# Optimization experiments

Hardware: AMD Instinct MI355X
Metric: run time of the kernel (lower is better)

The kernel has to match this reference:

```python
import jax, jax.numpy as jnp
import numpy as np


def setup_inputs() -> dict:
    key = jax.random.key(0)
    kx, kw = jax.random.split(key)
    x = jax.random.normal(kx, (32, 128, 8192), dtype=jnp.float32)
    weight = jax.random.normal(kw, (128, 128, 1, 2), dtype=jnp.float32)
    return {"x": x, "weight": weight}


def reference(x, weight):
    # x: (bs, cin, d); weight: (cout, cin, 1, 2)
    bs, cin, d = x.shape
    xp = x.reshape(bs, cin, d // 2, 2)          # (bs, cin, d/2, 2)
    w = weight[:, :, 0, :]                      # (cout, cin, 2)
    # out[b, o, p] = sum_{c,k} x[b,c,p,k] * w[o,c,k] / sqrt(cin)
    out = jnp.einsum('bcpk,ock->bop', xp, w) / jnp.sqrt(jnp.float32(cin))
    return out
```

## Files before the change

### kernel.cpp

```cpp
#include <hip/hip_runtime.h>
#include <stdint.h>


typedef __attribute__((ext_vector_type(8))) short bf16x8;
typedef __attribute__((ext_vector_type(4))) float f32x4;

#define CIN  128
#define DLEN 8192
#define PLEN 4096
#define COUT 128

__device__ inline unsigned short f2bf(float f) {
    unsigned u = __builtin_bit_cast(unsigned, f);
    unsigned r = u + 0x7FFFu + ((u >> 16) & 1u);
    return (unsigned short)(r >> 16);
}

__device__ inline unsigned pack_bf(float a, float b) {
    unsigned ua = __builtin_bit_cast(unsigned, a);
    unsigned ub = __builtin_bit_cast(unsigned, b);
    unsigned ra = ua + 0x7FFFu + ((ua >> 16) & 1u);
    unsigned rb = ub + 0x7FFFu + ((ub >> 16) & 1u);
    return (ra >> 16) | (rb & 0xFFFF0000u);
}

__global__ __launch_bounds__(256) void convert_w(const float* __restrict__ w,
                                                 unsigned short* __restrict__ wb) {
    int t  = blockIdx.x * 256 + threadIdx.x;
    int o  = t >> 7;
    int k0 = (t & 127) * 2;
    const float scale = 0.088388347648318447f;
    float2 f = *(const float2*)(w + o * 256 + k0);
    unsigned v = (unsigned)f2bf(f.x * scale) | ((unsigned)f2bf(f.y * scale) << 16);
    int idx = (k0 >> 3) * 1024 + o * 8 + (k0 & 7);
    *(unsigned*)(wb + idx) = v;
}

__global__ __launch_bounds__(256, 4) void conv_mfma(const float* __restrict__ x,
                                                    const unsigned short* __restrict__ wb,
                                                    float* __restrict__ out) {
    int tile = blockIdx.x;
    int b    = tile >> 5;
    int pt   = (tile & 31) * 128;
    int lane = threadIdx.x & 63;
    int w    = threadIdx.x >> 6;
    int quad = lane >> 4;
    int l16  = lane & 15;
    int pbase = pt + w * 32;

    const float* xl = x + (size_t)b * ((size_t)CIN * DLEN)
                        + (size_t)(quad * 4) * DLEN + 2 * pbase + 4 * l16;
    const uint32_t* bb = (const uint32_t*)wb + quad * 512 + l16 * 4;

    f32x4 acc[2][8];
#pragma unroll
    for (int mt = 0; mt < 2; ++mt)
#pragma unroll
        for (int t = 0; t < 8; ++t)
            acc[mt][t] = (f32x4)(0.0f);

    float4 abuf[4];
#pragma unroll
    for (int jj = 0; jj < 4; ++jj)
        abuf[jj] = *(const float4*)(xl + (size_t)jj * DLEN);

#pragma unroll 1
    for (int kc = 0; kc < 8; ++kc) {
        union { bf16x8 v; unsigned uu[4]; } afr0, afr1;
#pragma unroll
        for (int jj = 0; jj < 4; ++jj) {
            afr0.uu[jj] = pack_bf(abuf[jj].x, abuf[jj].y);
            afr1.uu[jj] = pack_bf(abuf[jj].z, abuf[jj].w);
        }
        if (kc < 7) {
            const float* nx = xl + (size_t)((kc + 1) * 16) * DLEN;
#pragma unroll
            for (int jj = 0; jj < 4; ++jj)
                abuf[jj] = *(const float4*)(nx + (size_t)jj * DLEN);
        }
        const uint32_t* bk = bb + kc * 2048;
#pragma unroll
        for (int th = 0; th < 2; ++th) {
            union { bf16x8 v; uint4 u; } bfr[4];
#pragma unroll
            for (int tt = 0; tt < 4; ++tt)
                bfr[tt].u = *(const uint4*)(bk + (th * 4 + tt) * 64);
#pragma unroll
            for (int tt = 0; tt < 4; ++tt) {
                int t = th * 4 + tt;
                acc[0][t] = __builtin_amdgcn_mfma_f32_16x16x32_bf16(afr0.v, bfr[tt].v, acc[0][t], 0, 0, 0);
                acc[1][t] = __builtin_amdgcn_mfma_f32_16x16x32_bf16(afr1.v, bfr[tt].v, acc[1][t], 0, 0, 0);
            }
        }
    }

    float* ob = out + (size_t)b * ((size_t)COUT * PLEN) + pbase + quad * 8;
#pragma unroll
    for (int t = 0; t < 8; ++t) {
        int o = t * 16 + l16;
        float* orow = ob + (size_t)o * PLEN;
        f32x4 v0 = { acc[0][t][0], acc[1][t][0], acc[0][t][1], acc[1][t][1] };
        f32x4 v1 = { acc[0][t][2], acc[1][t][2], acc[0][t][3], acc[1][t][3] };
        *(f32x4*)(orow)     = v0;
        *(f32x4*)(orow + 4) = v1;
    }
}

extern "C" void kernel_launch(void* const* d_in, const int* in_sizes, int n_in,
                              void* d_out, int out_size, void* d_ws, size_t ws_size,
                              hipStream_t stream) {
    const float* x = (const float*)d_in[0];
    const float* w = (const float*)d_in[1];
    float* out = (float*)d_out;
    unsigned short* wb = (unsigned short*)d_ws;

    convert_w<<<64, 256, 0, stream>>>(w, wb);
    conv_mfma<<<1024, 256, 0, stream>>>(x, wb, out);
}
```

Baseline: 212.6 us.

## Fuse weight conversion into conv kernel, stage bf16 weights in LDS

Drops the separate weight-conversion kernel launch. Each block now converts the full fp32 weight matrix to scaled bf16 and stores it in 64KB of shared memory, then reads B fragments from LDS instead of global memory. Blocks grow to 512 threads covering 256 positions, halving the grid to 512 blocks. This saves one launch and the global weight reads, but every block repeats the conversion, and the larger LDS footprint may limit how many blocks fit per CU.

```diff
diff --git a/kernel.cpp b/kernel.cpp
--- a/kernel.cpp
+++ b/kernel.cpp
@@ -24,24 +24,31 @@
     return (ra >> 16) | (rb & 0xFFFF0000u);
 }
 
-__global__ __launch_bounds__(256) void convert_w(const float* __restrict__ w,
-                                                 unsigned short* __restrict__ wb) {
-    int t  = blockIdx.x * 256 + threadIdx.x;
-    int o  = t >> 7;
-    int k0 = (t & 127) * 2;
+__global__ __launch_bounds__(512, 4) void conv_mfma(const float* __restrict__ x,
+                                                    const float* __restrict__ wsrc,
+                                                    float* __restrict__ out) {
+    __shared__ unsigned wlds[16384];
+
     const float scale = 0.088388347648318447f;
-    float2 f = *(const float2*)(w + o * 256 + k0);
-    unsigned v = (unsigned)f2bf(f.x * scale) | ((unsigned)f2bf(f.y * scale) << 16);
-    int idx = (k0 >> 3) * 1024 + o * 8 + (k0 & 7);
-    *(unsigned*)(wb + idx) = v;
-}
+#pragma unroll 4
+    for (int t = threadIdx.x; t < 4096; t += 512) {
+        int o  = t >> 5;
+        int k0 = (t & 31) * 8;
+        const float* wp = wsrc + o * 256 + k0;
+        float4 f0 = *(const float4*)(wp);
+        float4 f1 = *(const float4*)(wp + 4);
+        uint4 v;
+        v.x = pack_bf(f0.x * scale, f0.y * scale);
+        v.y = pack_bf(f0.z * scale, f0.w * scale);
+        v.z = pack_bf(f1.x * scale, f1.y * scale);
+        v.w = pack_bf(f1.z * scale, f1.w * scale);
+        *(uint4*)&wlds[(k0 >> 3) * 512 + o * 4] = v;
+    }
+    __syncthreads();
 
-__global__ __launch_bounds__(256, 4) void conv_mfma(const float* __restrict__ x,
-                                                    const unsigned short* __restrict__ wb,
-                                                    float* __restrict__ out) {
     int tile = blockIdx.x;
-    int b    = tile >> 5;
-    int pt   = (tile & 31) * 128;
+    int b    = tile >> 4;
+    int pt   = (tile & 15) * 256;
     int lane = threadIdx.x & 63;
     int w    = threadIdx.x >> 6;
     int quad = lane >> 4;
@@ -50,7 +57,7 @@
 
     const float* xl = x + (size_t)b * ((size_t)CIN * DLEN)
                         + (size_t)(quad * 4) * DLEN + 2 * pbase + 4 * l16;
-    const uint32_t* bb = (const uint32_t*)wb + quad * 512 + l16 * 4;
+    const unsigned* bb = wlds + quad * 512 + l16 * 4;
 
     f32x4 acc[2][8];
 #pragma unroll
@@ -78,7 +85,7 @@
             for (int jj = 0; jj < 4; ++jj)
                 abuf[jj] = *(const float4*)(nx + (size_t)jj * DLEN);
         }
-        const uint32_t* bk = bb + kc * 2048;
+        const unsigned* bk = bb + kc * 2048;
 #pragma unroll
         for (int th = 0; th < 2; ++th) {
             union { bf16x8 v; uint4 u; } bfr[4];
@@ -112,8 +119,7 @@
     const float* x = (const float*)d_in[0];
     const float* w = (const float*)d_in[1];
     float* out = (float*)d_out;
-    unsigned short* wb = (unsigned short*)d_ws;
+    (void)d_ws; (void)ws_size;
 
-    convert_w<<<64, 256, 0, stream>>>(w, wb);
-    conv_mfma<<<1024, 256, 0, stream>>>(x, wb, out);
+    conv_mfma<<<512, 512, 0, stream>>>(x, w, out);
 }
```

Measured after the change: 217.3 us. 1.02x slower.

## Stage weights in LDS via async loads, double-buffer x prefetch, use 512-thread blocks

Applied to the files above, without the earlier changes.

Each block now copies the whole 64KB bf16 weight matrix into shared memory with global_load_lds and reads B fragments from LDS instead of global memory. Blocks grow to 512 threads covering 256 positions, which halves the grid and amortizes the weight copy over more work. The x prefetch becomes two-deep, with two register buffers alternating between k-chunks to hide more global latency. The cost is 64KB of LDS per block, which limits occupancy, plus higher register pressure.

```diff
diff --git a/kernel.cpp b/kernel.cpp
--- a/kernel.cpp
+++ b/kernel.cpp
@@ -36,21 +36,36 @@
     *(unsigned*)(wb + idx) = v;
 }
 
-__global__ __launch_bounds__(256, 4) void conv_mfma(const float* __restrict__ x,
+__global__ __launch_bounds__(512, 4) void conv_mfma(const float* __restrict__ x,
                                                     const unsigned short* __restrict__ wb,
                                                     float* __restrict__ out) {
-    int tile = blockIdx.x;
-    int b    = tile >> 5;
-    int pt   = (tile & 31) * 128;
+    __shared__ unsigned wlds[16384];
+
     int lane = threadIdx.x & 63;
     int w    = threadIdx.x >> 6;
+
+    {
+        const char* gsrc = (const char*)wb + w * 1024 + lane * 16;
+        char* lbase = (char*)wlds + w * 1024;
+#pragma unroll
+        for (int i = 0; i < 8; ++i) {
+            __builtin_amdgcn_global_load_lds(
+                (const __attribute__((address_space(1))) void*)(gsrc + i * 8192),
+                (__attribute__((address_space(3))) void*)(lbase + i * 8192),
+                16, 0, 0);
+        }
+    }
+
+    int tile = blockIdx.x;
+    int b    = tile >> 4;
+    int pt   = (tile & 15) * 256;
     int quad = lane >> 4;
     int l16  = lane & 15;
     int pbase = pt + w * 32;
 
     const float* xl = x + (size_t)b * ((size_t)CIN * DLEN)
                         + (size_t)(quad * 4) * DLEN + 2 * pbase + 4 * l16;
-    const uint32_t* bb = (const uint32_t*)wb + quad * 512 + l16 * 4;
+    const unsigned* bb = wlds + quad * 512 + l16 * 4;
 
     f32x4 acc[2][8];
 #pragma unroll
@@ -59,40 +74,53 @@
         for (int t = 0; t < 8; ++t)
             acc[mt][t] = (f32x4)(0.0f);
 
-    float4 abuf[4];
+    float4 abufA[4], abufB[4];
 #pragma unroll
-    for (int jj = 0; jj < 4; ++jj)
-        abuf[jj] = *(const float4*)(xl + (size_t)jj * DLEN);
+    for (int jj = 0; jj < 4; ++jj) {
+        abufA[jj] = *(const float4*)(xl + (size_t)jj * DLEN);
+        abufB[jj] = *(const float4*)(xl + (size_t)(16 + jj) * DLEN);
+    }
+
+    __syncthreads();
+
+#define KC_BODY(KC, AB, PF)                                                        \
+    {                                                                              \
+        union { bf16x8 v; unsigned uu[4]; } afr0, afr1;                            \
+        _Pragma("unroll")                                                          \
+        for (int jj = 0; jj < 4; ++jj) {                                           \
+            afr0.uu[jj] = pack_bf(AB[jj].x, AB[jj].y);                             \
+            afr1.uu[jj] = pack_bf(AB[jj].z, AB[jj].w);                             \
+        }                                                                          \
+        if (PF) {                                                                  \
+            const float* nx = xl + (size_t)(((KC) + 2) * 16) * DLEN;               \
+            _Pragma("unroll")                                                      \
+            for (int jj = 0; jj < 4; ++jj)                                         \
+                AB[jj] = *(const float4*)(nx + (size_t)jj * DLEN);                 \
+        }                                                                          \
+        const unsigned* bk = bb + (KC) * 2048;                                     \
+        _Pragma("unroll")                                                          \
+        for (int th = 0; th < 2; ++th) {                                           \
+            union { bf16x8 v; uint4 u; } bfr[4];                                   \
+            _Pragma("unroll")                                                      \
+            for (int tt = 0; tt < 4; ++tt)                                         \
+                bfr[tt].u = *(const uint4*)(bk + (th * 4 + tt) * 64);              \
+            _Pragma("unroll")                                                      \
+            for (int tt = 0; tt < 4; ++tt) {                                       \
+                int t = th * 4 + tt;                                               \
+                acc[0][t] = __builtin_amdgcn_mfma_f32_16x16x32_bf16(afr0.v, bfr[tt].v, acc[0][t], 0, 0, 0); \
+                acc[1][t] = __builtin_amdgcn_mfma_f32_16x16x32_bf16(afr1.v, bfr[tt].v, acc[1][t], 0, 0, 0); \
+            }                                                                      \
+        }                                                                          \
+    }
 
 #pragma unroll 1
-    for (int kc = 0; kc < 8; ++kc) {
-        union { bf16x8 v; unsigned uu[4]; } afr0, afr1;
-#pragma unroll
-        for (int jj = 0; jj < 4; ++jj) {
-            afr0.uu[jj] = pack_bf(abuf[jj].x, abuf[jj].y);
-            afr1.uu[jj] = pack_bf(abuf[jj].z, abuf[jj].w);
-        }
-        if (kc < 7) {
-            const float* nx = xl + (size_t)((kc + 1) * 16) * DLEN;
-#pragma unroll
-            for (int jj = 0; jj < 4; ++jj)
-                abuf[jj] = *(const float4*)(nx + (size_t)jj * DLEN);
-        }
-        const uint32_t* bk = bb + kc * 2048;
-#pragma unroll
-        for (int th = 0; th < 2; ++th) {
-            union { bf16x8 v; uint4 u; } bfr[4];
-#pragma unroll
-            for (int tt = 0; tt < 4; ++tt)
-                bfr[tt].u = *(const uint4*)(bk + (th * 4 + tt) * 64);
-#pragma unroll
-            for (int tt = 0; tt < 4; ++tt) {
-                int t = th * 4 + tt;
-                acc[0][t] = __builtin_amdgcn_mfma_f32_16x16x32_bf16(afr0.v, bfr[tt].v, acc[0][t], 0, 0, 0);
-                acc[1][t] = __builtin_amdgcn_mfma_f32_16x16x32_bf16(afr1.v, bfr[tt].v, acc[1][t], 0, 0, 0);
-            }
-        }
+    for (int kc2 = 0; kc2 < 4; ++kc2) {
+        int kcA = kc2 * 2;
+        int kcB = kc2 * 2 + 1;
+        KC_BODY(kcA, abufA, (kc2 < 3));
+        KC_BODY(kcB, abufB, (kc2 < 3));
     }
+#undef KC_BODY
 
     float* ob = out + (size_t)b * ((size_t)COUT * PLEN) + pbase + quad * 8;
 #pragma unroll
@@ -115,5 +143,5 @@
     unsigned short* wb = (unsigned short*)d_ws;
 
     convert_w<<<64, 256, 0, stream>>>(w, wb);
-    conv_mfma<<<1024, 256, 0, stream>>>(x, wb, out);
+    conv_mfma<<<512, 512, 0, stream>>>(x, wb, out);
 }
```

After: 219.2 us. +3.1%, slower.
